# Kernel optimization log

Measured on AMD Instinct MI355X. Metric: run time of the kernel, lower is better.

Reference implementation:

```python
import jax, jax.numpy as jnp
import numpy as np

H, W = 16, 16
DIM = 512
HEADS = 8
DIM_HEAD = 64
INNER = HEADS * DIM_HEAD  # 512
B = 8
N = H * W  # 256
SCALE = DIM_HEAD ** -0.5
EPS = 1e-5


def _index_map(h, w):
    # index_map[n, m] = dx * (2w-1) + dy with dx = x-i+h-1, dy = y-j+w-1
    xs = np.arange(h)
    ys = np.arange(w)
    dx = xs[:, None] - xs[None, :] + h - 1            # (h, h)
    dy = ys[:, None] - ys[None, :] + w - 1            # (w, w)
    idx = dx[:, None, :, None] * (2 * w - 1) + dy[None, :, None, :]  # (h, w, h, w)
    return idx.reshape(h * w, h * w).astype(np.int32)


def setup_inputs() -> dict:
    key = jax.random.key(0)
    ks = jax.random.split(key, 5)
    x = jax.random.normal(ks[0], (B, N, DIM), dtype=jnp.float32)
    ln_g = jnp.ones((DIM,), jnp.float32)
    ln_b = jnp.zeros((DIM,), jnp.float32)
    w_qkv = jax.random.normal(ks[1], (DIM, 3 * INNER), jnp.float32) * 0.02
    unique_params = jax.random.normal(ks[2], ((2 * H - 1) * (2 * W - 1), INNER), jnp.float32) * 0.02
    w_out = jax.random.normal(ks[3], (INNER, DIM), jnp.float32) * 0.02
    b_out = jnp.zeros((DIM,), jnp.float32)
    idx_map = jnp.asarray(_index_map(H, W))  # (N, N) int32
    return {"x": x, "ln_g": ln_g, "ln_b": ln_b, "w_qkv": w_qkv,
            "unique_params": unique_params, "w_out": w_out, "b_out": b_out,
            "idx_map": idx_map}


def reference(x, ln_g, ln_b, w_qkv, unique_params, w_out, b_out, idx_map):
    b, n, _ = x.shape
    # LayerNorm
    mu = jnp.mean(x, axis=-1, keepdims=True)
    var = jnp.mean(jnp.square(x - mu), axis=-1, keepdims=True)
    xn = (x - mu) * jax.lax.rsqrt(var + EPS) * ln_g + ln_b
    # qkv projection (no bias)
    qkv = xn @ w_qkv                                  # (b, n, 3*inner)
    q, k, v = jnp.split(qkv, 3, axis=-1)
    q = q.reshape(b, n, HEADS, DIM_HEAD)
    k = k.reshape(b, n, HEADS, DIM_HEAD)
    v = v.reshape(b, n, HEADS, DIM_HEAD)
    # attention scores
    dots = jnp.einsum('bnhd,bmhd->bhnm', q, k) * SCALE
    attn = jax.nn.softmax(dots, axis=-1)              # (b, h, n, m)
    # relative-position table: (n, m, h, d)
    rpos = unique_params[idx_map].reshape(n, n, HEADS, DIM_HEAD)
    # out[b,h,n,d] = sum_m attn[b,h,n,m] * (v[b,m,h,d] + rpos[n,m,h,d])
    out = jnp.einsum('bhnm,bmhd->bnhd', attn, v) \
        + jnp.einsum('bhnm,nmhd->bnhd', attn, rpos)
    out = out.reshape(b, n, INNER)
    return out @ w_out + b_out
```

## Files before the change

kernel.cpp:

```cpp
#include <hip/hip_runtime.h>
#include <math.h>

#define NB 8
#define SEQ 256
#define DIMC 512
#define NHEAD 8
#define DHEAD 64
#define SCALEF 0.125f

typedef __attribute__((ext_vector_type(8))) short s16x8;
typedef __attribute__((ext_vector_type(4))) float f32x4;

typedef __attribute__((address_space(3))) unsigned int lds_u32_t;
typedef const __attribute__((address_space(1))) unsigned int g_u32_t;
static __device__ __forceinline__ void gl_lds16(const void* gsrc, void* ldst) {
  __builtin_amdgcn_global_load_lds((g_u32_t*)gsrc, (lds_u32_t*)ldst, 16, 0, 0);
}

static __device__ __forceinline__ unsigned short f2bf(float f) {
  union { float f; unsigned u; } c; c.f = f;
  unsigned r = c.u + 0x7FFF + ((c.u >> 16) & 1);
  return (unsigned short)(r >> 16);
}

static __device__ void tcast_body(const float* __restrict__ W,
    unsigned short* __restrict__ WT, int K, int N, int n0, int k0, int t,
    float (*tile)[65]) {
#pragma unroll
  for (int i = 0; i < 16; ++i) {
    const int idx = i * 256 + t;
    const int kl = idx >> 6, nl = idx & 63;
    tile[kl][nl] = W[(size_t)(k0 + kl) * N + n0 + nl];
  }
  __syncthreads();
#pragma unroll
  for (int i = 0; i < 16; ++i) {
    const int idx = i * 256 + t;
    const int nl = idx >> 6, kl = idx & 63;
    WT[(size_t)(n0 + nl) * K + k0 + kl] = f2bf(tile[kl][nl]);
  }
}

__global__ __launch_bounds__(256) void prep_kernel(const float* __restrict__ x,
    const float* __restrict__ g, const float* __restrict__ bta,
    const float* __restrict__ w_qkv, const float* __restrict__ w_out,
    const float* __restrict__ up, unsigned short* __restrict__ xnb,
    unsigned short* __restrict__ wqt, unsigned short* __restrict__ wot,
    unsigned short* __restrict__ upT) {
  __shared__ float tile[64][65];
  __shared__ float sh_s[4], sh_q[4];
  const int t = threadIdx.x;
  const int bid = blockIdx.x;
  if (bid < 192) {
    tcast_body(w_qkv, wqt, 512, 1536, (bid % 24) * 64, (bid / 24) * 64, t, tile);
  } else if (bid < 256) {
    const int b2 = bid - 192;
    tcast_body(w_out, wot, 512, 512, (b2 % 8) * 64, (b2 / 8) * 64, t, tile);
  } else if (bid < 384) {
    const int b2 = bid - 256;
    const int k0 = (b2 >> 3) * 64, n0 = (b2 & 7) * 64;
#pragma unroll
    for (int i = 0; i < 16; ++i) {
      const int idx = i * 256 + t;
      const int kl = idx >> 6, nl = idx & 63;
      const int k = k0 + kl;
      tile[kl][nl] = (k < 961) ? up[(size_t)k * 512 + n0 + nl] : 0.0f;
    }
    __syncthreads();
#pragma unroll
    for (int i = 0; i < 16; ++i) {
      const int idx = i * 256 + t;
      const int nl = idx >> 6, kl = idx & 63;
      if (k0 + kl < 992)
        upT[(size_t)(n0 + nl) * 992 + k0 + kl] = f2bf(tile[kl][nl]);
    }
  } else {
    const int row = bid - 384;
    const float2 v = ((const float2*)(x + (size_t)row * DIMC))[t];
    float s = v.x + v.y;
    float q = v.x * v.x + v.y * v.y;
#pragma unroll
    for (int off = 32; off > 0; off >>= 1) {
      s += __shfl_down(s, off);
      q += __shfl_down(q, off);
    }
    const int wave = t >> 6, lane = t & 63;
    if (lane == 0) { sh_s[wave] = s; sh_q[wave] = q; }
    __syncthreads();
    const float fs = sh_s[0] + sh_s[1] + sh_s[2] + sh_s[3];
    const float fq = sh_q[0] + sh_q[1] + sh_q[2] + sh_q[3];
    const float mean = fs * (1.0f / DIMC);
    const float inv = rsqrtf(fq * (1.0f / DIMC) - mean * mean + 1e-5f);
    const float2 gv = ((const float2*)g)[t];
    const float2 bv = ((const float2*)bta)[t];
    ushort2 o;
    o.x = f2bf((v.x - mean) * inv * gv.x + bv.x);
    o.y = f2bf((v.y - mean) * inv * gv.y + bv.y);
    ((ushort2*)(xnb + (size_t)row * DIMC))[t] = o;
  }
}

template <int BM, int BN, bool BIAS, bool OUTBF, bool VSPLIT>
__global__ __launch_bounds__(256) void mfma_gemm_bt(
    const unsigned short* __restrict__ A, const unsigned short* __restrict__ BT,
    const float* __restrict__ bias, void* __restrict__ Cv,
    unsigned short* __restrict__ vtb, int M, int K, int N) {
  constexpr int TR = BM / 32;
  constexpr int TC = BN / 32;
  __shared__ unsigned short As[BM * 32];
  __shared__ unsigned short Bs[BN * 32];
  const int t = threadIdx.x;
  const int wave = t >> 6, lane = t & 63;
  const int wr = wave >> 1, wc = wave & 1;
  const int bm = blockIdx.x * BM, bn = blockIdx.y * BN;

  f32x4 acc[TR][TC] = {};

  const int fr = lane & 15, q4 = lane >> 4;
  const int kBlocks = K >> 5;
  for (int kb = 0; kb < kBlocks; ++kb) {
    const int k0 = kb << 5;
    __syncthreads();
#pragma unroll
    for (int c = 0; c < (BM * 4 + 255) / 256; ++c) {
      const int p = c * 256 + t;
      if (BM * 4 % 256 == 0 || p < BM * 4) {
        const int row = p >> 2;
        const int jl = (p & 3) ^ ((row >> 1) & 3);
        gl_lds16(A + (size_t)(bm + row) * K + k0 + jl * 8,
                 As + (size_t)(c * 256 + wave * 64) * 8);
      }
    }
#pragma unroll
    for (int c = 0; c < (BN * 4 + 255) / 256; ++c) {
      const int p = c * 256 + t;
      if (BN * 4 % 256 == 0 || p < BN * 4) {
        const int row = p >> 2;
        const int jl = (p & 3) ^ ((row >> 1) & 3);
        gl_lds16(BT + (size_t)(bn + row) * K + k0 + jl * 8,
                 Bs + (size_t)(c * 256 + wave * 64) * 8);
      }
    }
    __syncthreads();
    s16x8 af[TR], bfr[TC];
#pragma unroll
    for (int i = 0; i < TR; ++i) {
      const int row = wr * (BM / 2) + i * 16 + fr;
      const int jp = q4 ^ ((row >> 1) & 3);
      af[i] = *(const s16x8*)(As + row * 32 + jp * 8);
    }
#pragma unroll
    for (int j = 0; j < TC; ++j) {
      const int row = wc * (BN / 2) + j * 16 + fr;
      const int jp = q4 ^ ((row >> 1) & 3);
      bfr[j] = *(const s16x8*)(Bs + row * 32 + jp * 8);
    }
#pragma unroll
    for (int i = 0; i < TR; ++i)
#pragma unroll
      for (int j = 0; j < TC; ++j)
        acc[i][j] = __builtin_amdgcn_mfma_f32_16x16x32_bf16(af[i], bfr[j],
                                                            acc[i][j], 0, 0, 0);
  }
  if (VSPLIT && bn >= 1024) {
#pragma unroll
    for (int i = 0; i < TR; ++i) {
#pragma unroll
      for (int j = 0; j < TC; ++j) {
        const int hc = bn - 1024 + wc * (BN / 2) + j * 16 + fr;
        const int h = hc >> 6, d = hc & 63;
#pragma unroll
        for (int r = 0; r < 4; ++r) {
          const int row = bm + wr * (BM / 2) + i * 16 + q4 * 4 + r;
          const int b = row >> 8, m = row & 255;
          vtb[(size_t)((b * 8 + h) * 64 + d) * 256 + m] = f2bf(acc[i][j][r]);
        }
      }
    }
    return;
  }
#pragma unroll
  for (int i = 0; i < TR; ++i) {
#pragma unroll
    for (int j = 0; j < TC; ++j) {
      const int col = bn + wc * (BN / 2) + j * 16 + fr;
      const float bv = BIAS ? bias[col] : 0.0f;
#pragma unroll
      for (int r = 0; r < 4; ++r) {
        const int row = bm + wr * (BM / 2) + i * 16 + q4 * 4 + r;
        if constexpr (OUTBF) {
          ((unsigned short*)Cv)[(size_t)row * N + col] = f2bf(acc[i][j][r] + bv);
        } else {
          ((float*)Cv)[(size_t)row * N + col] = acc[i][j][r] + bv;
        }
      }
    }
  }
}

#define PSTR 264
#define ASTR2 520
__global__ __launch_bounds__(256) void attn_rpos_kernel(
    const unsigned short* __restrict__ qkvb,
    const unsigned short* __restrict__ vtb,
    const unsigned short* __restrict__ upT,
    unsigned short* __restrict__ ob) {
  __shared__ unsigned short ascat[16 * ASTR2];
  __shared__ unsigned short p_lds[16 * PSTR];
  __shared__ float smax[4][16], ssum[4][16];
  const int bh = blockIdx.y, b = bh >> 3, h = bh & 7;
  const int xn = blockIdx.x;
  const int n0 = xn * 16;
  const int t = threadIdx.x, wave = t >> 6, lane = t & 63;
  const int fr = lane & 15, q4 = lane >> 4;
  const int kwin0 = (xn * 31) & ~7;

  {
    const s16x8 z = {0, 0, 0, 0, 0, 0, 0, 0};
#pragma unroll
    for (int i = 0; i < 5; ++i) {
      const int idx = i * 256 + t;
      if (idx < 16 * ASTR2 / 8) *(s16x8*)(ascat + idx * 8) = z;
    }
  }

  s16x8 qf[2];
  {
    const size_t qrow = (size_t)(b * SEQ + n0 + fr) * 1536 + h * 64;
#pragma unroll
    for (int ks = 0; ks < 2; ++ks)
      qf[ks] = *(const s16x8*)(qkvb + qrow + ks * 32 + q4 * 8);
  }

  f32x4 s[4];
#pragma unroll
  for (int j = 0; j < 4; ++j) s[j] = (f32x4){0.f, 0.f, 0.f, 0.f};
  {
    const unsigned short* kb =
        qkvb + (size_t)(b * SEQ + wave * 64 + fr) * 1536 + 512 + h * 64;
#pragma unroll
    for (int ks = 0; ks < 2; ++ks)
#pragma unroll
      for (int j = 0; j < 4; ++j) {
        const s16x8 kf =
            *(const s16x8*)(kb + (size_t)j * (16 * 1536) + ks * 32 + q4 * 8);
        s[j] = __builtin_amdgcn_mfma_f32_16x16x32_bf16(qf[ks], kf, s[j], 0, 0, 0);
      }
  }

  float mx[4] = {-1e30f, -1e30f, -1e30f, -1e30f};
#pragma unroll
  for (int j = 0; j < 4; ++j)
#pragma unroll
    for (int r = 0; r < 4; ++r) {
      s[j][r] *= SCALEF;
      mx[r] = fmaxf(mx[r], s[j][r]);
    }
#pragma unroll
  for (int r = 0; r < 4; ++r) {
    mx[r] = fmaxf(mx[r], __shfl_xor(mx[r], 1));
    mx[r] = fmaxf(mx[r], __shfl_xor(mx[r], 2));
    mx[r] = fmaxf(mx[r], __shfl_xor(mx[r], 4));
    mx[r] = fmaxf(mx[r], __shfl_xor(mx[r], 8));
  }
  if (fr == 0) {
#pragma unroll
    for (int r = 0; r < 4; ++r) smax[wave][q4 * 4 + r] = mx[r];
  }
  __syncthreads();

  float fm[4];
#pragma unroll
  for (int r = 0; r < 4; ++r) {
    const int row = q4 * 4 + r;
    fm[r] = fmaxf(fmaxf(smax[0][row], smax[1][row]),
                  fmaxf(smax[2][row], smax[3][row]));
  }
  float sum[4] = {0.f, 0.f, 0.f, 0.f};
#pragma unroll
  for (int j = 0; j < 4; ++j)
#pragma unroll
    for (int r = 0; r < 4; ++r) {
      s[j][r] = __expf(s[j][r] - fm[r]);
      sum[r] += s[j][r];
    }
#pragma unroll
  for (int r = 0; r < 4; ++r) {
    sum[r] += __shfl_xor(sum[r], 1);
    sum[r] += __shfl_xor(sum[r], 2);
    sum[r] += __shfl_xor(sum[r], 4);
    sum[r] += __shfl_xor(sum[r], 8);
  }
  if (fr == 0) {
#pragma unroll
    for (int r = 0; r < 4; ++r) ssum[wave][q4 * 4 + r] = sum[r];
  }
  __syncthreads();

  float invs[4];
#pragma unroll
  for (int r = 0; r < 4; ++r) {
    const int row = q4 * 4 + r;
    invs[r] = 1.0f / (ssum[0][row] + ssum[1][row] + ssum[2][row] + ssum[3][row]);
  }

#pragma unroll
  for (int j = 0; j < 4; ++j) {
    const int mt = wave * 4 + j;
#pragma unroll
    for (int r = 0; r < 4; ++r) {
      const int row = q4 * 4 + r;
      const unsigned short pb = f2bf(s[j][r] * invs[r]);
      p_lds[row * PSTR + mt * 16 + fr] = pb;
      const int c = (xn - mt + 15) * 31 + (row - fr + 15) - kwin0;
      ascat[row * ASTR2 + c] = pb;
    }
  }
  __syncthreads();

  f32x4 oA = (f32x4){0.f, 0.f, 0.f, 0.f}, oB = oA, oC = oA, oD = oA;
  {
    const unsigned short* uB =
        upT + (size_t)(h * 64 + wave * 16 + fr) * 992 + kwin0;
    const unsigned short* aR = ascat + fr * ASTR2;
#pragma unroll
    for (int ks = 0; ks < 8; ++ks) {
      const s16x8 af = *(const s16x8*)(aR + ks * 32 + q4 * 8);
      const s16x8 bfg = *(const s16x8*)(uB + ks * 32 + q4 * 8);
      oA = __builtin_amdgcn_mfma_f32_16x16x32_bf16(af, bfg, oA, 0, 0, 0);
    }
#pragma unroll
    for (int ks = 8; ks < 16; ++ks) {
      const s16x8 af = *(const s16x8*)(aR + ks * 32 + q4 * 8);
      const s16x8 bfg = *(const s16x8*)(uB + ks * 32 + q4 * 8);
      oB = __builtin_amdgcn_mfma_f32_16x16x32_bf16(af, bfg, oB, 0, 0, 0);
    }
  }
  {
    const unsigned short* vB = vtb + (size_t)(bh * 64 + wave * 16 + fr) * 256;
    const unsigned short* pR = p_lds + fr * PSTR;
#pragma unroll
    for (int ks = 0; ks < 4; ++ks) {
      const s16x8 pf = *(const s16x8*)(pR + ks * 32 + q4 * 8);
      const s16x8 vfg = *(const s16x8*)(vB + ks * 32 + q4 * 8);
      oC = __builtin_amdgcn_mfma_f32_16x16x32_bf16(pf, vfg, oC, 0, 0, 0);
    }
#pragma unroll
    for (int ks = 4; ks < 8; ++ks) {
      const s16x8 pf = *(const s16x8*)(pR + ks * 32 + q4 * 8);
      const s16x8 vfg = *(const s16x8*)(vB + ks * 32 + q4 * 8);
      oD = __builtin_amdgcn_mfma_f32_16x16x32_bf16(pf, vfg, oD, 0, 0, 0);
    }
  }
  const f32x4 o = (oA + oB) + (oC + oD);
#pragma unroll
  for (int r = 0; r < 4; ++r) {
    const int n = n0 + q4 * 4 + r;
    ob[(size_t)(b * SEQ + n) * DIMC + h * 64 + wave * 16 + fr] = f2bf(o[r]);
  }
}

extern "C" void kernel_launch(void* const* d_in, const int* in_sizes, int n_in,
                              void* d_out, int out_size, void* d_ws,
                              size_t ws_size, hipStream_t stream) {
  const float* x = (const float*)d_in[0];
  const float* ln_g = (const float*)d_in[1];
  const float* ln_b = (const float*)d_in[2];
  const float* w_qkv = (const float*)d_in[3];
  const float* up = (const float*)d_in[4];
  const float* w_out = (const float*)d_in[5];
  const float* b_out = (const float*)d_in[6];
  float* out = (float*)d_out;

  unsigned short* u = (unsigned short*)d_ws;
  unsigned short* qkvb = u;
  unsigned short* xnb = u + 3145728;
  unsigned short* ob = u + 4194304;
  unsigned short* wqt = u + 5242880;
  unsigned short* wot = u + 6029312;
  unsigned short* upT = u + 6291456;
  unsigned short* vtb = u + 6799360;
  if (ws_size < (size_t)7847936 * sizeof(unsigned short)) return;

  prep_kernel<<<2432, 256, 0, stream>>>(x, ln_g, ln_b, w_qkv, w_out, up,
                                        xnb, wqt, wot, upT);
  mfma_gemm_bt<64, 64, false, true, true>
      <<<dim3(32, 24), 256, 0, stream>>>(xnb, wqt, nullptr, qkvb, vtb,
                                         2048, 512, 1536);
  attn_rpos_kernel<<<dim3(16, 64), 256, 0, stream>>>(qkvb, vtb, upT, ob);
  mfma_gemm_bt<64, 32, true, false, false>
      <<<dim3(32, 16), 256, 0, stream>>>(ob, wot, b_out, out, nullptr,
                                         2048, 512, 512);
}
```

Measured before the change: 111.3 us.

## Double-buffer GEMM LDS tiles and widen K-step to 64

The bf16 MFMA GEMM now uses two LDS buffers per operand and prefetches the next K tile with async global-to-LDS loads while the current tile is computed. Each iteration also covers a K depth of 64 instead of 32, with an 8-way XOR swizzle, which halves the number of barrier-separated iterations. The aim is to hide global load latency and cut synchronisation overhead in the QKV and output projections. In exchange LDS use quadruples, which may lower occupancy, and the loop assumes K is a multiple of 64 and that BM*8 and BN*8 are multiples of 256.

New measurement: 108.2 us. 1.03x faster.

```diff
diff --git a/kernel.cpp b/kernel.cpp
--- a/kernel.cpp
+++ b/kernel.cpp
@@ -107,61 +107,73 @@
     unsigned short* __restrict__ vtb, int M, int K, int N) {
   constexpr int TR = BM / 32;
   constexpr int TC = BN / 32;
-  __shared__ unsigned short As[BM * 32];
-  __shared__ unsigned short Bs[BN * 32];
+  __shared__ unsigned short As[2][BM * 64];
+  __shared__ unsigned short Bs[2][BN * 64];
   const int t = threadIdx.x;
   const int wave = t >> 6, lane = t & 63;
   const int wr = wave >> 1, wc = wave & 1;
   const int bm = blockIdx.x * BM, bn = blockIdx.y * BN;
+  const int fr = lane & 15, q4 = lane >> 4;
 
   f32x4 acc[TR][TC] = {};
 
-  const int fr = lane & 15, q4 = lane >> 4;
-  const int kBlocks = K >> 5;
-  for (int kb = 0; kb < kBlocks; ++kb) {
-    const int k0 = kb << 5;
+  const int nk = K >> 6;
+
+#define STAGE_TILE(sel, kb)                                                   \
+  {                                                                           \
+    const int k0s = (kb) << 6;                                                \
+    _Pragma("unroll")                                                         \
+    for (int c = 0; c < BM * 8 / 256; ++c) {                                  \
+      const int p = c * 256 + t;                                              \
+      const int row = p >> 3;                                                 \
+      const int so = (p & 7) ^ (row & 7);                                     \
+      gl_lds16(A + (size_t)(bm + row) * K + k0s + so * 8,                     \
+               &As[sel][(size_t)(c * 256 + wave * 64) * 8]);                  \
+    }                                                                         \
+    _Pragma("unroll")                                                         \
+    for (int c = 0; c < BN * 8 / 256; ++c) {                                  \
+      const int p = c * 256 + t;                                              \
+      const int row = p >> 3;                                                 \
+      const int so = (p & 7) ^ (row & 7);                                     \
+      gl_lds16(BT + (size_t)(bn + row) * K + k0s + so * 8,                    \
+               &Bs[sel][(size_t)(c * 256 + wave * 64) * 8]);                  \
+    }                                                                         \
+  }
+
+  STAGE_TILE(0, 0);
+  __syncthreads();
+  int cur = 0;
+  for (int kb = 0; kb < nk; ++kb) {
+    if (kb + 1 < nk) STAGE_TILE(cur ^ 1, kb + 1);
+    s16x8 af[2][TR], bfr[2][TC];
+#pragma unroll
+    for (int ks = 0; ks < 2; ++ks) {
+#pragma unroll
+      for (int i = 0; i < TR; ++i) {
+        const int row = wr * (BM / 2) + i * 16 + fr;
+        const int op = (ks * 4 + q4) ^ (row & 7);
+        af[ks][i] = *(const s16x8*)(&As[cur][row * 64 + op * 8]);
+      }
+#pragma unroll
+      for (int j = 0; j < TC; ++j) {
+        const int row = wc * (BN / 2) + j * 16 + fr;
+        const int op = (ks * 4 + q4) ^ (row & 7);
+        bfr[ks][j] = *(const s16x8*)(&Bs[cur][row * 64 + op * 8]);
+      }
+    }
+#pragma unroll
+    for (int ks = 0; ks < 2; ++ks)
+#pragma unroll
+      for (int i = 0; i < TR; ++i)
+#pragma unroll
+        for (int j = 0; j < TC; ++j)
+          acc[i][j] = __builtin_amdgcn_mfma_f32_16x16x32_bf16(
+              af[ks][i], bfr[ks][j], acc[i][j], 0, 0, 0);
     __syncthreads();
-#pragma unroll
-    for (int c = 0; c < (BM * 4 + 255) / 256; ++c) {
-      const int p = c * 256 + t;
-      if (BM * 4 % 256 == 0 || p < BM * 4) {
-        const int row = p >> 2;
-        const int jl = (p & 3) ^ ((row >> 1) & 3);
-        gl_lds16(A + (size_t)(bm + row) * K + k0 + jl * 8,
-                 As + (size_t)(c * 256 + wave * 64) * 8);
-      }
-    }
-#pragma unroll
-    for (int c = 0; c < (BN * 4 + 255) / 256; ++c) {
-      const int p = c * 256 + t;
-      if (BN * 4 % 256 == 0 || p < BN * 4) {
-        const int row = p >> 2;
-        const int jl = (p & 3) ^ ((row >> 1) & 3);
-        gl_lds16(BT + (size_t)(bn + row) * K + k0 + jl * 8,
-                 Bs + (size_t)(c * 256 + wave * 64) * 8);
-      }
-    }
-    __syncthreads();
-    s16x8 af[TR], bfr[TC];
-#pragma unroll
-    for (int i = 0; i < TR; ++i) {
-      const int row = wr * (BM / 2) + i * 16 + fr;
-      const int jp = q4 ^ ((row >> 1) & 3);
-      af[i] = *(const s16x8*)(As + row * 32 + jp * 8);
-    }
-#pragma unroll
-    for (int j = 0; j < TC; ++j) {
-      const int row = wc * (BN / 2) + j * 16 + fr;
-      const int jp = q4 ^ ((row >> 1) & 3);
-      bfr[j] = *(const s16x8*)(Bs + row * 32 + jp * 8);
-    }
-#pragma unroll
-    for (int i = 0; i < TR; ++i)
-#pragma unroll
-      for (int j = 0; j < TC; ++j)
-        acc[i][j] = __builtin_amdgcn_mfma_f32_16x16x32_bf16(af[i], bfr[j],
-                                                            acc[i][j], 0, 0, 0);
-  }
+    cur ^= 1;
+  }
+#undef STAGE_TILE
+
   if (VSPLIT && bn >= 1024) {
 #pragma unroll
     for (int i = 0; i < TR; ++i) {
```
